# Optimization experiments

Hardware: AMD Instinct MI355X
Metric: run time of the kernel (lower is better)

The kernel has to match this reference:

```python
import jax, jax.numpy as jnp
import numpy as np

B, C, H, W = 4, 512, 64, 64
CA = C // 2  # attention hidden channels


def _conv1x1(x, w):
    # w: [O, I], x: [B, I, H, W]
    return jnp.einsum('oi,bihw->bohw', w, x)


def _conv3x3(x, w, b):
    y = jax.lax.conv_general_dilated(x, w, (1, 1), 'SAME',
                                     dimension_numbers=('NCHW', 'OIHW', 'NCHW'))
    return y + b[None, :, None, None]


def _scan_dir(x, w, b, axis, reverse):
    # IRNN recurrence along `axis`: prev = relu(prev * w + b + x_t), per-channel w,b.
    # The boundary position (first in scan order after un-flipping) stays zero,
    # matching the torch code which never writes it.
    xs = jnp.moveaxis(x, axis, 0)          # [L, B, C, other]
    if reverse:
        xs = xs[::-1]
    wb = w.reshape(1, -1, 1)
    bb = b.reshape(1, -1, 1)

    def step(prev, xt):
        new = jax.nn.relu(prev * wb + bb + xt)
        return new, new

    init = jax.nn.relu(xs[0])
    _, ys = jax.lax.scan(step, init, xs[1:])
    ys = jnp.concatenate([jnp.zeros_like(ys[:1]), ys], axis=0)
    if reverse:
        ys = ys[::-1]
    return jnp.moveaxis(ys, 0, axis)


def _irnn(x, wu, wr, wd, wl, bu, br, bd, bl):
    up = _scan_dir(x, wu, bu, 2, True)     # scans from bottom row upward
    right = _scan_dir(x, wr, br, 3, False)
    down = _scan_dir(x, wd, bd, 2, False)
    left = _scan_dir(x, wl, bl, 3, True)
    return up, right, down, left


def setup_inputs() -> dict:
    key = jax.random.key(0)
    ks = jax.random.split(key, 32)

    def n(k, shape, scale):
        return jax.random.normal(k, shape, jnp.float32) * scale

    inp = {
        'x': n(ks[0], (B, C, H, W), 1.0),
        # Attention: conv3x3(C->C/2)+b, conv3x3(C/2->C/2)+b, conv1x1(C/2->4)+b
        'a_w1': n(ks[1], (CA, C, 3, 3), (C * 9) ** -0.5),
        'a_b1': n(ks[2], (CA,), 0.02),
        'a_w2': n(ks[3], (CA, CA, 3, 3), (CA * 9) ** -0.5),
        'a_b2': n(ks[4], (CA,), 0.02),
        'a_w3': n(ks[5], (4, CA, 1, 1), CA ** -0.5),
        'a_b3': n(ks[6], (4,), 0.02),
        'cin_w': n(ks[7], (C, C), C ** -0.5),   # conv_in 1x1, bias=False
        'c2_w': n(ks[8], (C, 4 * C), (4 * C) ** -0.5),
        'c3_w': n(ks[9], (C, 4 * C), (4 * C) ** -0.5),
    }
    # IRNN per-channel recurrence weights (alpha=1.0 init) and biases
    i = 10
    for tag in ('i1', 'i2'):
        for d in ('u', 'r', 'd', 'l'):
            inp[f'{tag}_w{d}'] = jnp.ones((C,), jnp.float32)
            inp[f'{tag}_b{d}'] = n(ks[i], (C,), 0.05)
            i += 1
    return inp


def reference(x, a_w1, a_b1, a_w2, a_b2, a_w3, a_b3, cin_w,
              i1_wu, i1_bu, i1_wr, i1_br, i1_wd, i1_bd, i1_wl, i1_bl,
              c2_w,
              i2_wu, i2_bu, i2_wr, i2_br, i2_wd, i2_bd, i2_wl, i2_bl,
              c3_w):
    # Attention branch — computed but NEVER applied: the original torch code
    # uses out-of-place .mul() and discards the result (faithful reproduction).
    a = jax.nn.relu(_conv3x3(x, a_w1, a_b1))
    a = jax.nn.relu(_conv3x3(a, a_w2, a_b2))
    _weight = jax.nn.sigmoid(_conv1x1(a, a_w3[:, :, 0, 0]) + a_b3[None, :, None, None])

    out = _conv1x1(x, cin_w)
    u, r, d, l = _irnn(out, i1_wu, i1_wr, i1_wd, i1_wl, i1_bu, i1_br, i1_bd, i1_bl)
    out = jnp.concatenate([u, r, d, l], axis=1)   # [B, 4C, H, W]
    out = _conv1x1(out, c2_w)
    u, r, d, l = _irnn(out, i2_wu, i2_wr, i2_wd, i2_wl, i2_bu, i2_br, i2_bd, i2_bl)
    out = jnp.concatenate([u, r, d, l], axis=1)
    out = jax.nn.relu(_conv1x1(out, c3_w))
    return out
```

## Files before the change

kernel.cpp:

```cpp
#include <hip/hip_runtime.h>
#include <stdint.h>

#define NB 4
#define CB 512
#define HH 64
#define WW 64
#define HW 4096
#define C4 2048
#define PTOT (NB*HW)

typedef float  f32x4  __attribute__((ext_vector_type(4)));
typedef short  bf16x8 __attribute__((ext_vector_type(8)));

__device__ __forceinline__ float relu_f(float v){ return v > 0.f ? v : 0.f; }

__device__ __forceinline__ float bf2f(unsigned short u){
    union { uint32_t i; float f; } v; v.i = ((uint32_t)u) << 16; return v.f;
}
__device__ __forceinline__ unsigned short f2bf(float f){
    union { float f; uint32_t i; } v; v.f = f;
    uint32_t r = v.i + 0x7FFFu + ((v.i >> 16) & 1u);
    return (unsigned short)(r >> 16);
}

__device__ __forceinline__ void gload16(const void* g, void* l){
    __builtin_amdgcn_global_load_lds(
        (const __attribute__((address_space(1))) uint32_t*)g,
        (__attribute__((address_space(3))) uint32_t*)l, 16, 0, 0);
}

__global__ __launch_bounds__(256) void cast3_f32_bf16(
    const float* __restrict__ a, unsigned short* __restrict__ oa,
    const float* __restrict__ b, unsigned short* __restrict__ ob,
    const float* __restrict__ c, unsigned short* __restrict__ oc)
{
    int i = blockIdx.x * 256 + threadIdx.x;
    const float* src; unsigned short* dst; int j;
    if (i < 65536)        { src = a; dst = oa; j = i; }
    else if (i < 327680)  { src = b; dst = ob; j = i - 65536; }
    else                  { src = c; dst = oc; j = i - 327680; }
    float4 v = ((const float4*)src)[j];
    ushort4 o;
    o.x = f2bf(v.x); o.y = f2bf(v.y); o.z = f2bf(v.z); o.w = f2bf(v.w);
    ((ushort4*)dst)[j] = o;
}

__global__ __launch_bounds__(256) void transpose_cast_x(
    const float* __restrict__ x, unsigned short* __restrict__ xT)
{
    __shared__ unsigned short tile[64][72];
    const int b  = blockIdx.z;
    const int p0 = blockIdx.x * 64;
    const int c0 = blockIdx.y * 64;
    const int t  = threadIdx.x;

    const int pl = (t & 15) * 4;
    const int cl = t >> 4;
    const float* src = x + ((size_t)b * CB + c0) * HW + p0;
    #pragma unroll
    for (int r = 0; r < 4; r++) {
        int c = cl + r * 16;
        float4 v = *(const float4*)(src + (size_t)c * HW + pl);
        tile[pl + 0][c] = f2bf(v.x);
        tile[pl + 1][c] = f2bf(v.y);
        tile[pl + 2][c] = f2bf(v.z);
        tile[pl + 3][c] = f2bf(v.w);
    }
    __syncthreads();
    unsigned short* dst = xT + ((size_t)b * HW + p0) * CB + c0;
    const int cl2 = (t & 15) * 4;
    const int pl2 = t >> 4;
    #pragma unroll
    for (int r = 0; r < 4; r++) {
        int p = pl2 + r * 16;
        ushort4 o = *(ushort4*)&tile[p][cl2];
        *(ushort4*)(dst + (size_t)p * CB + cl2) = o;
    }
}

template<int K, int OUTMODE>
__global__ __launch_bounds__(512) __attribute__((amdgpu_waves_per_eu(1, 2)))
void gemm_cl(
    const unsigned short* __restrict__ A,
    const unsigned short* __restrict__ Bw,
    void* __restrict__ out)
{
    extern __shared__ __align__(16) char lds[];

    const int t    = threadIdx.x;
    const int lane = t & 63;
    const int wid  = t >> 6;
    const int p0   = blockIdx.x * 128;
    const int o0   = blockIdx.y * 256;

    const int l15 = lane & 15;
    const int l4  = lane >> 4;
    const int wm  = (wid >> 2) * 64;
    const int wn  = (wid & 3) * 64;
    const int swz = (l15 & 7) << 4;

    f32x4 acc[4][4];
    #pragma unroll
    for (int m = 0; m < 4; m++)
        #pragma unroll
        for (int n = 0; n < 4; n++) acc[m][n] = (f32x4)0.f;

    const int sr  = lane >> 3;
    const int scb = (lane & 7) * 16;
    const int skk = (scb ^ (sr << 4)) >> 1;

    auto STAGE = [&](int k0, int bufo) {
        #pragma unroll
        for (int j = 0; j < 2; ++j)
            gload16(A + (size_t)(p0 + j * 64 + wid * 8 + sr) * K + k0 + skk,
                    lds + bufo + j * 8192 + wid * 1024);
        #pragma unroll
        for (int j = 0; j < 4; ++j)
            gload16(Bw + (size_t)(o0 + j * 64 + wid * 8 + sr) * K + k0 + skk,
                    lds + bufo + 16384 + j * 8192 + wid * 1024);
    };

    STAGE(0, 0);
    const int NT = K / 64;

#define PH(khv, mhv, STCODE)                                                   \
    {                                                                          \
        const int colb = (khv) * 64 + l4 * 16;                                 \
        af0 = *(const bf16x8*)(lds + co + (wm + (2*(mhv)  )*16 + l15)*128 + (colb ^ swz)); \
        af1 = *(const bf16x8*)(lds + co + (wm + (2*(mhv)+1)*16 + l15)*128 + (colb ^ swz)); \
        if ((mhv) == 0) {                                                      \
            _Pragma("unroll")                                                  \
            for (int nn = 0; nn < 4; ++nn)                                     \
                bfr[nn] = *(const bf16x8*)(lds + co + 16384 +                  \
                           (wn + nn*16 + l15)*128 + (colb ^ swz));             \
        }                                                                      \
        STCODE;                                                                \
        __builtin_amdgcn_sched_barrier(0);                                     \
        __builtin_amdgcn_s_barrier();                                          \
        asm volatile("s_waitcnt lgkmcnt(0)" ::: "memory");                     \
        __builtin_amdgcn_sched_barrier(0);                                     \
        __builtin_amdgcn_s_setprio(1);                                         \
        _Pragma("unroll")                                                      \
        for (int nn = 0; nn < 4; ++nn) {                                       \
            acc[2*(mhv)  ][nn] = __builtin_amdgcn_mfma_f32_16x16x32_bf16(      \
                                    af0, bfr[nn], acc[2*(mhv)  ][nn], 0, 0, 0);\
            acc[2*(mhv)+1][nn] = __builtin_amdgcn_mfma_f32_16x16x32_bf16(      \
                                    af1, bfr[nn], acc[2*(mhv)+1][nn], 0, 0, 0);\
        }                                                                      \
        __builtin_amdgcn_s_setprio(0);                                         \
        __builtin_amdgcn_sched_barrier(0);                                     \
        __builtin_amdgcn_s_barrier();                                          \
    }

    #pragma unroll 1
    for (int tt = 0; tt < NT; ++tt) {
        const int co = (tt & 1) * 49152;
        const int no = 49152 - co;
        asm volatile("s_waitcnt vmcnt(0)" ::: "memory");
        __builtin_amdgcn_s_barrier();
        const bool st = (tt + 1 < NT);
        const int k1 = (tt + 1) * 64;
        bf16x8 bfr[4], af0, af1;

        PH(0, 0, { if (st) STAGE(k1, no); })
        PH(0, 1, { })
        PH(1, 0, { })
        PH(1, 1, { })
    }
#undef PH

    if (OUTMODE == 0) {
        unsigned short* op = (unsigned short*)out;
        #pragma unroll
        for (int m = 0; m < 4; m++)
            #pragma unroll
            for (int r = 0; r < 4; r++) {
                const int p = p0 + wm + m * 16 + l4 * 4 + r;
                #pragma unroll
                for (int n = 0; n < 4; n++) {
                    const int o = o0 + wn + n * 16 + l15;
                    op[(size_t)p * CB + o] = f2bf(acc[m][n][r]);
                }
            }
    } else {
        __syncthreads();
        float (*tl)[132] = (float(*)[132])lds;
        const int bb   = p0 >> 12;
        const int phw0 = p0 & (HW - 1);
        #pragma unroll
        for (int h = 0; h < 2; ++h) {
            if (((wid >> 1) & 1) == h) {
                #pragma unroll
                for (int n = 0; n < 4; n++)
                    #pragma unroll
                    for (int m = 0; m < 4; m++)
                        #pragma unroll
                        for (int r = 0; r < 4; r++)
                            tl[(wn & 127) + n * 16 + l15][wm + m * 16 + l4 * 4 + r]
                                = acc[m][n][r];
            }
            __syncthreads();
            const int orow = t >> 2;
            const int pseg = (t & 3) * 32;
            float* dst = (float*)out +
                ((size_t)(bb * CB + o0 + h * 128 + orow)) * HW + phw0 + pseg;
            #pragma unroll
            for (int j = 0; j < 8; j++) {
                float4 v = *(float4*)&tl[orow][pseg + j * 4];
                v.x = relu_f(v.x); v.y = relu_f(v.y); v.z = relu_f(v.z); v.w = relu_f(v.w);
                *(float4*)(dst + j * 4) = v;
            }
            __syncthreads();
        }
    }
}

__global__ __launch_bounds__(256) void irnn_fused(
    const unsigned short* __restrict__ in, unsigned short* __restrict__ outc,
    const float* __restrict__ wu, const float* __restrict__ bu,
    const float* __restrict__ wr, const float* __restrict__ br,
    const float* __restrict__ wd, const float* __restrict__ bd,
    const float* __restrict__ wl, const float* __restrict__ bl)
{
    const int dir = blockIdx.y;
    const float* wv; const float* bv; int pstep, rev;
    if      (dir == 0) { wv = wu; bv = bu; pstep = 64; rev = 1; }
    else if (dir == 1) { wv = wr; bv = br; pstep = 1;  rev = 0; }
    else if (dir == 2) { wv = wd; bv = bd; pstep = 64; rev = 0; }
    else               { wv = wl; bv = bl; pstep = 1;  rev = 1; }
    const int dirOff = dir * 512;

    const int idx = blockIdx.x * 256 + threadIdx.x;
    const int c = idx & 511;
    const int f = (idx >> 9) & 63;
    const int b = idx >> 15;
    const int fbase = (pstep == 64) ? f : f * 64;

    const float wc = wv[c], bc = bv[c];
    const int t0 = rev ? 63 : 0;
    const int dp = rev ? -pstep : pstep;
    const int istep = dp * CB;
    const int ostep = dp * C4;

    const unsigned short* ip = in   + ((size_t)b * HW + fbase + (size_t)t0 * pstep) * CB + c;
    unsigned short*       op = outc + ((size_t)b * HW + fbase + (size_t)t0 * pstep) * C4 + dirOff + c;

    float s = relu_f(bf2f(ip[0]));
    op[0] = 0;

    unsigned short v0 = ip[1*istep], v1 = ip[2*istep], v2 = ip[3*istep], v3 = ip[4*istep],
                   v4 = ip[5*istep], v5 = ip[6*istep], v6 = ip[7*istep], v7 = ip[8*istep];

#define DO(kk, vv) { s = relu_f(fmaf(s, wc, bc + bf2f(vv))); op[(kk)*ostep] = f2bf(s); }
    for (int g = 0; g < 6; ++g) {
        const int k0 = 1 + 8 * g;
        DO(k0+0, v0); v0 = ip[(k0+ 8)*istep];
        DO(k0+1, v1); v1 = ip[(k0+ 9)*istep];
        DO(k0+2, v2); v2 = ip[(k0+10)*istep];
        DO(k0+3, v3); v3 = ip[(k0+11)*istep];
        DO(k0+4, v4); v4 = ip[(k0+12)*istep];
        DO(k0+5, v5); v5 = ip[(k0+13)*istep];
        DO(k0+6, v6); v6 = ip[(k0+14)*istep];
        DO(k0+7, v7); v7 = ip[(k0+15)*istep];
    }
    DO(49, v0); v0 = ip[57*istep];
    DO(50, v1); v1 = ip[58*istep];
    DO(51, v2); v2 = ip[59*istep];
    DO(52, v3); v3 = ip[60*istep];
    DO(53, v4); v4 = ip[61*istep];
    DO(54, v5); v5 = ip[62*istep];
    DO(55, v6); v6 = ip[63*istep];
    DO(56, v7);
    DO(57, v0); DO(58, v1); DO(59, v2); DO(60, v3);
    DO(61, v4); DO(62, v5); DO(63, v6);
#undef DO
}

extern "C" void kernel_launch(void* const* d_in, const int* in_sizes, int n_in,
                              void* d_out, int out_size, void* d_ws, size_t ws_size,
                              hipStream_t stream) {
    const float* x     = (const float*)d_in[0];
    const float* cin_w = (const float*)d_in[7];
    const float* c2_w  = (const float*)d_in[8];
    const float* c3_w  = (const float*)d_in[9];
    const float* i1_wu = (const float*)d_in[10];
    const float* i1_bu = (const float*)d_in[11];
    const float* i1_wr = (const float*)d_in[12];
    const float* i1_br = (const float*)d_in[13];
    const float* i1_wd = (const float*)d_in[14];
    const float* i1_bd = (const float*)d_in[15];
    const float* i1_wl = (const float*)d_in[16];
    const float* i1_bl = (const float*)d_in[17];
    const float* i2_wu = (const float*)d_in[18];
    const float* i2_bu = (const float*)d_in[19];
    const float* i2_wr = (const float*)d_in[20];
    const float* i2_br = (const float*)d_in[21];
    const float* i2_wd = (const float*)d_in[22];
    const float* i2_bd = (const float*)d_in[23];
    const float* i2_wl = (const float*)d_in[24];
    const float* i2_bl = (const float*)d_in[25];

    char* ws = (char*)d_ws;
    unsigned short* xT     = (unsigned short*)(ws);
    unsigned short* concat = (unsigned short*)(ws + (size_t)16 * 1024 * 1024);
    unsigned short* mid    = (unsigned short*)(ws + (size_t)80 * 1024 * 1024);
    unsigned short* wA     = (unsigned short*)(ws + (size_t)96 * 1024 * 1024);
    unsigned short* wB     = (unsigned short*)(wA + 512 * 512);
    unsigned short* wC     = (unsigned short*)(wB + 512 * 2048);

    cast3_f32_bf16<<<2304, 256, 0, stream>>>(cin_w, wA, c2_w, wB, c3_w, wC);
    transpose_cast_x<<<dim3(HW/64, CB/64, NB), 256, 0, stream>>>(x, xT);

    dim3 ggrid(PTOT/128, CB/256);
    dim3 sgrid(512, 4);
    const size_t GEMM_LDS = 98304;

    gemm_cl<512, 0><<<ggrid, 512, GEMM_LDS, stream>>>(xT, wA, mid);

    irnn_fused<<<sgrid, 256, 0, stream>>>(mid, concat,
        i1_wu, i1_bu, i1_wr, i1_br, i1_wd, i1_bd, i1_wl, i1_bl);

    gemm_cl<2048, 0><<<ggrid, 512, GEMM_LDS, stream>>>(concat, wB, mid);

    irnn_fused<<<sgrid, 256, 0, stream>>>(mid, concat,
        i2_wu, i2_bu, i2_wr, i2_br, i2_wd, i2_bd, i2_wl, i2_bl);

    gemm_cl<2048, 1><<<ggrid, 512, GEMM_LDS, stream>>>(concat, wC, d_out);
}
```

Measured before the change: 157.6 us.

## Triple-buffer GEMM LDS pipeline with split staging and swizzled block order

```diff
diff --git a/kernel.cpp b/kernel.cpp
--- a/kernel.cpp
+++ b/kernel.cpp
@@ -79,7 +79,7 @@
 }
 
 template<int K, int OUTMODE>
-__global__ __launch_bounds__(512) __attribute__((amdgpu_waves_per_eu(1, 2)))
+__global__ __launch_bounds__(512) __attribute__((amdgpu_waves_per_eu(2, 2)))
 void gemm_cl(
     const unsigned short* __restrict__ A,
     const unsigned short* __restrict__ Bw,
@@ -90,8 +90,11 @@
     const int t    = threadIdx.x;
     const int lane = t & 63;
     const int wid  = t >> 6;
-    const int p0   = blockIdx.x * 128;
-    const int o0   = blockIdx.y * 256;
+
+    const int lin = blockIdx.x + (int)gridDim.x * blockIdx.y;
+    const int vl  = (lin & 7) * 32 + (lin >> 3);
+    const int p0  = (vl >> 1) * 128;
+    const int o0  = (vl & 1) * 256;
 
     const int l15 = lane & 15;
     const int l4  = lane >> 4;
@@ -109,65 +112,68 @@
     const int scb = (lane & 7) * 16;
     const int skk = (scb ^ (sr << 4)) >> 1;
 
-    auto STAGE = [&](int k0, int bufo) {
-        #pragma unroll
-        for (int j = 0; j < 2; ++j)
-            gload16(A + (size_t)(p0 + j * 64 + wid * 8 + sr) * K + k0 + skk,
-                    lds + bufo + j * 8192 + wid * 1024);
-        #pragma unroll
-        for (int j = 0; j < 4; ++j)
-            gload16(Bw + (size_t)(o0 + j * 64 + wid * 8 + sr) * K + k0 + skk,
-                    lds + bufo + 16384 + j * 8192 + wid * 1024);
+    auto STAGE3 = [&](int k0, int bufo, int part) {
+        if (part == 0) {
+            #pragma unroll
+            for (int j = 0; j < 2; ++j)
+                gload16(A + (size_t)(p0 + j * 64 + wid * 8 + sr) * K + k0 + skk,
+                        lds + bufo + j * 8192 + wid * 1024);
+            gload16(Bw + (size_t)(o0 + wid * 8 + sr) * K + k0 + skk,
+                    lds + bufo + 16384 + wid * 1024);
+        } else {
+            #pragma unroll
+            for (int j = 1; j < 4; ++j)
+                gload16(Bw + (size_t)(o0 + j * 64 + wid * 8 + sr) * K + k0 + skk,
+                        lds + bufo + 16384 + j * 8192 + wid * 1024);
+        }
     };
 
-    STAGE(0, 0);
-    const int NT = K / 64;
-
-#define PH(khv, mhv, STCODE)                                                   \
+#define PHASE(khv, part, dost, k2v, fov)                                       \
     {                                                                          \
         const int colb = (khv) * 64 + l4 * 16;                                 \
-        af0 = *(const bf16x8*)(lds + co + (wm + (2*(mhv)  )*16 + l15)*128 + (colb ^ swz)); \
-        af1 = *(const bf16x8*)(lds + co + (wm + (2*(mhv)+1)*16 + l15)*128 + (colb ^ swz)); \
-        if ((mhv) == 0) {                                                      \
-            _Pragma("unroll")                                                  \
-            for (int nn = 0; nn < 4; ++nn)                                     \
-                bfr[nn] = *(const bf16x8*)(lds + co + 16384 +                  \
-                           (wn + nn*16 + l15)*128 + (colb ^ swz));             \
-        }                                                                      \
-        STCODE;                                                                \
-        __builtin_amdgcn_sched_barrier(0);                                     \
-        __builtin_amdgcn_s_barrier();                                          \
+        bf16x8 af[4], bf[4];                                                   \
+        _Pragma("unroll")                                                      \
+        for (int m = 0; m < 4; ++m)                                            \
+            af[m] = *(const bf16x8*)(lds + co + (wm + m * 16 + l15) * 128      \
+                                     + (colb ^ swz));                          \
+        _Pragma("unroll")                                                      \
+        for (int n = 0; n < 4; ++n)                                            \
+            bf[n] = *(const bf16x8*)(lds + co + 16384 +                        \
+                                     (wn + n * 16 + l15) * 128 + (colb ^ swz));\
+        if (dost) STAGE3(k2v, fov, part);                                      \
         asm volatile("s_waitcnt lgkmcnt(0)" ::: "memory");                     \
         __builtin_amdgcn_sched_barrier(0);                                     \
         __builtin_amdgcn_s_setprio(1);                                         \
         _Pragma("unroll")                                                      \
-        for (int nn = 0; nn < 4; ++nn) {                                       \
-            acc[2*(mhv)  ][nn] = __builtin_amdgcn_mfma_f32_16x16x32_bf16(      \
-                                    af0, bfr[nn], acc[2*(mhv)  ][nn], 0, 0, 0);\
-            acc[2*(mhv)+1][nn] = __builtin_amdgcn_mfma_f32_16x16x32_bf16(      \
-                                    af1, bfr[nn], acc[2*(mhv)+1][nn], 0, 0, 0);\
-        }                                                                      \
+        for (int m = 0; m < 4; ++m)                                            \
+            _Pragma("unroll")                                                  \
+            for (int n = 0; n < 4; ++n)                                        \
+                acc[m][n] = __builtin_amdgcn_mfma_f32_16x16x32_bf16(           \
+                                af[m], bf[n], acc[m][n], 0, 0, 0);             \
         __builtin_amdgcn_s_setprio(0);                                         \
         __builtin_amdgcn_sched_barrier(0);                                     \
-        __builtin_amdgcn_s_barrier();                                          \
-    }
-
+    }
+
+    const int NT = K / 64;
+    STAGE3(0, 0, 0);      STAGE3(0, 0, 1);
+    STAGE3(64, 49152, 0); STAGE3(64, 49152, 1);
+
+    int co = 0, no_ = 49152, fo = 98304;
     #pragma unroll 1
     for (int tt = 0; tt < NT; ++tt) {
-        const int co = (tt & 1) * 49152;
-        const int no = 49152 - co;
-        asm volatile("s_waitcnt vmcnt(0)" ::: "memory");
+        if (tt < NT - 1) asm volatile("s_waitcnt vmcnt(6)" ::: "memory");
+        else             asm volatile("s_waitcnt vmcnt(0)" ::: "memory");
         __builtin_amdgcn_s_barrier();
-        const bool st = (tt + 1 < NT);
-        const int k1 = (tt + 1) * 64;
-        bf16x8 bfr[4], af0, af1;
-
-        PH(0, 0, { if (st) STAGE(k1, no); })
-        PH(0, 1, { })
-        PH(1, 0, { })
-        PH(1, 1, { })
-    }
-#undef PH
+        const bool st = (tt + 2 < NT);
+        const int k2  = (tt + 2) * 64;
+
+        PHASE(0, 0, st, k2, fo)
+        __builtin_amdgcn_s_barrier();
+        PHASE(1, 1, st, k2, fo)
+
+        const int tmp = co; co = no_; no_ = fo; fo = tmp;
+    }
+#undef PHASE
 
     if (OUTMODE == 0) {
         unsigned short* op = (unsigned short*)out;
@@ -313,7 +319,7 @@
 
     dim3 ggrid(PTOT/128, CB/256);
     dim3 sgrid(512, 4);
-    const size_t GEMM_LDS = 98304;
+    const size_t GEMM_LDS = 147456;
 
     gemm_cl<512, 0><<<ggrid, 512, GEMM_LDS, stream>>>(xT, wA, mid);
 
```

Result: faster. 148.0 us (-6.1%).
